# Optimization experiments

Hardware: AMD Instinct MI355X
Metric: run time of the kernel (lower is better)

Reference implementation:

```python
import jax, jax.numpy as jnp
import numpy as np

N, HW, CI = 16, 16384, 2
DIM, DEPTH, CO = 256, 4, 3
OMEGA = 30.0
E = CI * DIM + DIM + DEPTH * (DIM * DIM + DIM)  # 263936


def setup_inputs() -> dict:
    key = jax.random.key(0)
    ks = jax.random.split(key, 8)
    x = jax.random.normal(ks[0], (N, HW, CI), jnp.float32)
    weight_offset = jax.random.normal(ks[1], (N, E), jnp.float32) * 0.01
    # layer 0: uniform(-1/ch_in, 1/ch_in); hidden: uniform(-sqrt(6/dim), sqrt(6/dim)); biases zero
    v0 = 1.0 / CI
    w0 = jax.random.uniform(ks[2], (CI, DIM), jnp.float32, -v0, v0)
    b0 = jnp.zeros((DIM,), jnp.float32)
    vh = float(np.sqrt(6.0 / DIM))
    ws_h = jax.random.uniform(ks[3], (DEPTH, DIM, DIM), jnp.float32, -vh, vh)
    bs_h = jnp.zeros((DEPTH, DIM), jnp.float32)
    # output Linear (torch default init bound 1/sqrt(fan_in)); stored as [DIM, CO]
    lim = float(1.0 / np.sqrt(DIM))
    w_out = jax.random.uniform(ks[4], (DIM, CO), jnp.float32, -lim, lim)
    b_out = jax.random.uniform(ks[5], (CO,), jnp.float32, -lim, lim)
    out_scale = jnp.ones((CO,), jnp.float32)  # output_scale coeff = 1.0
    return {"x": x, "weight_offset": weight_offset, "w0": w0, "b0": b0,
            "ws_h": ws_h, "bs_h": bs_h, "w_out": w_out, "b_out": b_out,
            "out_scale": out_scale}


def reference(x, weight_offset, w0, b0, ws_h, bs_h, w_out, b_out, out_scale):
    n = x.shape[0]
    i = CI * DIM
    ow0 = weight_offset[:, :i].reshape(n, CI, DIM)      # [N, CI, DIM]
    ob0 = weight_offset[:, i:i + DIM]                   # [N, DIM]
    i += DIM
    # first layer: per-sample weight = base + offset, then sin(omega * .)
    h = jnp.einsum('nhc,ncd->nhd', x, w0[None] + ow0) + (b0[None] + ob0)[:, None, :]
    h = jnp.sin(OMEGA * h)
    for l in range(DEPTH):
        ow = weight_offset[:, i:i + DIM * DIM].reshape(n, DIM, DIM)
        i += DIM * DIM
        ob = weight_offset[:, i:i + DIM]
        i += DIM
        h = jnp.einsum('nhd,nde->nhe', h, ws_h[l][None] + ow) + (bs_h[l][None] + ob)[:, None, :]
        h = jnp.sin(h)
    return (h @ w_out + b_out) * out_scale
```

## Files before the change

kernel.cpp:

```cpp
#include <hip/hip_runtime.h>


#define N_S 16
#define HW_S 16384
#define E_S 263936
#define INV2PI 0.15915494309189535f
#define OM2PI  4.774648292756860f

typedef _Float16 f16x8 __attribute__((ext_vector_type(8)));
typedef _Float16 f16x4 __attribute__((ext_vector_type(4)));
typedef _Float16 f16x2 __attribute__((ext_vector_type(2)));
typedef float f32x4 __attribute__((ext_vector_type(4)));

#define WT_OFF   0u
#define W0T_OFF  8388608u
#define B0_OFF   8421376u
#define BE_OFF   8437760u

__device__ __forceinline__ float fsin(float z) {
  return __builtin_amdgcn_sinf(__builtin_amdgcn_fractf(z));
}

__global__ __launch_bounds__(256) void siren_pre(
    const float* __restrict__ wo, const float* __restrict__ w0,
    const float* __restrict__ b0, const float* __restrict__ wsh,
    const float* __restrict__ bsh, char* __restrict__ ws)
{
  __shared__ float tile[64][65];
  int b = blockIdx.x, t = threadIdx.x;
  if (b < 1024) {
    int n = b >> 6, rem = b & 63, l = rem >> 4, sub = rem & 15;
    int tk = sub >> 2, te = sub & 3;
    int e_loc = t & 63, ksub = t >> 6;
    const float* wo_n = wo + (size_t)n * E_S + 768 + l * 65792;
    const float* wsh_l = wsh + l * 65536;
    for (int r = 0; r < 16; ++r) {
      int k_loc = ksub * 16 + r;
      int k = tk * 64 + k_loc, e = te * 64 + e_loc;
      tile[k_loc][e_loc] = (wsh_l[k * 256 + e] + wo_n[k * 256 + e]) * INV2PI;
    }
    __syncthreads();
    _Float16* wtl = (_Float16*)(ws + WT_OFF) + (size_t)(n * 4 + l) * 65536;
    int kp = (t & 31) * 2, esub = t >> 5;
    for (int r = 0; r < 8; ++r) {
      int e_loc2 = esub * 8 + r;
      f16x2 hv;
      hv[0] = (_Float16)tile[kp][e_loc2];
      hv[1] = (_Float16)tile[kp + 1][e_loc2];
      int e = te * 64 + e_loc2, k = tk * 64 + kp;
      int c = k >> 5, kin = k & 31;
      *(f16x2*)(wtl + (size_t)c * 8192 + e * 32 + kin) = hv;
    }
  } else if (b == 1024) {
    float* w0t = (float*)(ws + W0T_OFF);
    float* b0e = (float*)(ws + B0_OFF);
    for (int idx = t; idx < 4096; idx += 256) {
      int n = idx >> 8, e = idx & 255;
      const float* wo_n = wo + (size_t)n * E_S;
      float2 v;
      v.x = (w0[e] + wo_n[e]) * OM2PI;
      v.y = (w0[256 + e] + wo_n[256 + e]) * OM2PI;
      *(float2*)(w0t + (n * 256 + e) * 2) = v;
      b0e[n * 256 + e] = (b0[e] + wo_n[512 + e]) * OM2PI;
    }
  } else {
    float* be = (float*)(ws + BE_OFF);
    for (int idx = t; idx < 16384; idx += 256) {
      int n = idx >> 10, rem = idx & 1023, l = rem >> 8, e = rem & 255;
      be[(n * 4 + l) * 256 + e] =
          (bsh[l * 256 + e] + wo[(size_t)n * E_S + 768 + l * 65792 + 65536 + e]) * INV2PI;
    }
  }
}

__global__ __launch_bounds__(256, 2) void siren_main(
    const float* __restrict__ x, const char* __restrict__ ws,
    const float* __restrict__ w_out, const float* __restrict__ b_out,
    const float* __restrict__ out_scale, float* __restrict__ out)
{
  __shared__ __align__(16) unsigned char sH[65536];
  __shared__ float sWf[768];
  __shared__ float sRed[2][128][3];
  __shared__ float sFin[384];

  int tid = threadIdx.x;
  int lane = tid & 63, wave = tid >> 6;
  int g = lane >> 4, li = lane & 15;
  int we = wave & 1, wp = wave >> 1;
  int bid = blockIdx.x;
  int n = bid & 15, tile = bid >> 4;

  const char* wt_n = ws + WT_OFF + (size_t)n * 524288;

  for (int i = tid; i < 768; i += 256) sWf[i] = w_out[i];

  {
    const float* xp = x + ((size_t)n * HW_S + (size_t)tile * 128) * 2;
    int p = tid & 127;
    float2 xv = *(const float2*)(xp + p * 2);
    const float* w0t = (const float*)(ws + W0T_OFF) + n * 512;
    const float* b0e = (const float*)(ws + B0_OFF) + n * 256;
    int swz = (p & 7) << 4;
    unsigned char* hrow = sH + p * 512;
#pragma unroll
    for (int it = 0; it < 16; ++it) {
      int eg = (tid >> 7) * 16 + it;
      int e0 = eg * 8;
      f32x4 wa = *(const f32x4*)(w0t + e0 * 2);
      f32x4 wb = *(const f32x4*)(w0t + e0 * 2 + 4);
      f32x4 wc = *(const f32x4*)(w0t + e0 * 2 + 8);
      f32x4 wd = *(const f32x4*)(w0t + e0 * 2 + 12);
      f32x4 ba = *(const f32x4*)(b0e + e0);
      f32x4 bb = *(const f32x4*)(b0e + e0 + 4);
      f16x8 hv;
      hv[0] = (_Float16)fsin(fmaf(xv.y, wa[1], fmaf(xv.x, wa[0], ba[0])));
      hv[1] = (_Float16)fsin(fmaf(xv.y, wa[3], fmaf(xv.x, wa[2], ba[1])));
      hv[2] = (_Float16)fsin(fmaf(xv.y, wb[1], fmaf(xv.x, wb[0], ba[2])));
      hv[3] = (_Float16)fsin(fmaf(xv.y, wb[3], fmaf(xv.x, wb[2], ba[3])));
      hv[4] = (_Float16)fsin(fmaf(xv.y, wc[1], fmaf(xv.x, wc[0], bb[0])));
      hv[5] = (_Float16)fsin(fmaf(xv.y, wc[3], fmaf(xv.x, wc[2], bb[1])));
      hv[6] = (_Float16)fsin(fmaf(xv.y, wd[1], fmaf(xv.x, wd[0], bb[2])));
      hv[7] = (_Float16)fsin(fmaf(xv.y, wd[3], fmaf(xv.x, wd[2], bb[3])));
      *(f16x8*)(hrow + ((eg * 16) ^ swz)) = hv;
    }
  }
  __syncthreads();

  const float* be_n = (const float*)(ws + BE_OFF) + n * 1024;
  int laneoff = (we * 128 + li) * 64 + g * 16;
  f32x4 acc[8][4];

  for (int l = 0; l < 4; ++l) {
    const float* bias = be_n + l * 256;
#pragma unroll
    for (int et = 0; et < 8; ++et) {
      f32x4 bv = *(const f32x4*)(bias + we * 128 + et * 16 + g * 4);
#pragma unroll
      for (int pt = 0; pt < 4; ++pt) acc[et][pt] = bv;
    }
    const char* wl = wt_n + (size_t)l * 131072 + laneoff;
#pragma unroll
    for (int c = 0; c < 8; ++c) {
      f16x8 afr[8], bfr[4];
#pragma unroll
      for (int et = 0; et < 8; ++et)
        afr[et] = *(const f16x8*)(wl + c * 16384 + et * 1024);
#pragma unroll
      for (int pt = 0; pt < 4; ++pt) {
        int p = wp * 64 + pt * 16 + li;
        bfr[pt] = *(const f16x8*)(sH + p * 512 + ((c * 64 + g * 16) ^ ((p & 7) << 4)));
      }
#pragma unroll
      for (int et = 0; et < 8; ++et)
#pragma unroll
        for (int pt = 0; pt < 4; ++pt)
          acc[et][pt] = __builtin_amdgcn_mfma_f32_16x16x32_f16(afr[et], bfr[pt], acc[et][pt], 0, 0, 0);
    }
    if (l < 3) {
      __syncthreads();
#pragma unroll
      for (int et = 0; et < 8; ++et) {
        int eb = we * 256 + et * 32 + g * 8;
#pragma unroll
        for (int pt = 0; pt < 4; ++pt) {
          int p = wp * 64 + pt * 16 + li;
          f16x4 hv;
#pragma unroll
          for (int r = 0; r < 4; ++r)
            hv[r] = (_Float16)fsin(acc[et][pt][r]);
          *(f16x4*)(sH + p * 512 + (eb ^ ((p & 7) << 4))) = hv;
        }
      }
      __syncthreads();
    }
  }

  float part[4][3];
#pragma unroll
  for (int pt = 0; pt < 4; ++pt)
#pragma unroll
    for (int co = 0; co < 3; ++co) part[pt][co] = 0.f;
#pragma unroll
  for (int et = 0; et < 8; ++et) {
#pragma unroll
    for (int r = 0; r < 4; ++r) {
      int e = we * 128 + et * 16 + g * 4 + r;
      float wc0 = sWf[e * 3 + 0], wc1 = sWf[e * 3 + 1], wc2 = sWf[e * 3 + 2];
#pragma unroll
      for (int pt = 0; pt < 4; ++pt) {
        float h = fsin(acc[et][pt][r]);
        part[pt][0] = fmaf(h, wc0, part[pt][0]);
        part[pt][1] = fmaf(h, wc1, part[pt][1]);
        part[pt][2] = fmaf(h, wc2, part[pt][2]);
      }
    }
  }
#pragma unroll
  for (int pt = 0; pt < 4; ++pt)
#pragma unroll
    for (int co = 0; co < 3; ++co) {
      float v = part[pt][co];
      v += __shfl_xor(v, 16);
      v += __shfl_xor(v, 32);
      part[pt][co] = v;
    }
  if (g == 0) {
#pragma unroll
    for (int pt = 0; pt < 4; ++pt) {
      int p = wp * 64 + pt * 16 + li;
#pragma unroll
      for (int co = 0; co < 3; ++co)
        sRed[we][p][co] = part[pt][co];
    }
  }
  __syncthreads();
  if (tid < 128) {
    int p = tid;
#pragma unroll
    for (int co = 0; co < 3; ++co)
      sFin[p * 3 + co] = (sRed[0][p][co] + sRed[1][p][co] +
                          b_out[co]) * out_scale[co];
  }
  __syncthreads();
  float* op = out + ((size_t)n * HW_S + (size_t)tile * 128) * 3;
  for (int i = tid; i < 384; i += 256) op[i] = sFin[i];
}

extern "C" void kernel_launch(void* const* d_in, const int* in_sizes, int n_in,
                              void* d_out, int out_size, void* d_ws, size_t ws_size,
                              hipStream_t stream) {
  const float* x      = (const float*)d_in[0];
  const float* wo     = (const float*)d_in[1];
  const float* w0     = (const float*)d_in[2];
  const float* b0     = (const float*)d_in[3];
  const float* wsh    = (const float*)d_in[4];
  const float* bsh    = (const float*)d_in[5];
  const float* w_out  = (const float*)d_in[6];
  const float* b_out  = (const float*)d_in[7];
  const float* oscale = (const float*)d_in[8];
  float* out = (float*)d_out;
  char* ws = (char*)d_ws;

  siren_pre<<<1026, 256, 0, stream>>>(wo, w0, b0, wsh, bsh, ws);
  siren_main<<<2048, 256, 0, stream>>>(x, ws, w_out, b_out, oscale, out);
}
```

Measured before the change: 200.5 us.

## Switch hidden layers to 32x32x16 MFMA with per-wave output-column split

```diff
diff --git a/kernel.cpp b/kernel.cpp
--- a/kernel.cpp
+++ b/kernel.cpp
@@ -11,6 +11,7 @@
 typedef _Float16 f16x4 __attribute__((ext_vector_type(4)));
 typedef _Float16 f16x2 __attribute__((ext_vector_type(2)));
 typedef float f32x4 __attribute__((ext_vector_type(4)));
+typedef float f32x16 __attribute__((ext_vector_type(16)));
 
 #define WT_OFF   0u
 #define W0T_OFF  8388608u
@@ -80,13 +81,12 @@
 {
   __shared__ __align__(16) unsigned char sH[65536];
   __shared__ float sWf[768];
-  __shared__ float sRed[2][128][3];
+  __shared__ float sRed[4][128][3];
   __shared__ float sFin[384];
 
   int tid = threadIdx.x;
-  int lane = tid & 63, wave = tid >> 6;
-  int g = lane >> 4, li = lane & 15;
-  int we = wave & 1, wp = wave >> 1;
+  int lane = tid & 63, eq = tid >> 6;
+  int l31 = lane & 31, lh = lane >> 5;
   int bid = blockIdx.x;
   int n = bid & 15, tile = bid >> 4;
 
@@ -100,7 +100,7 @@
     float2 xv = *(const float2*)(xp + p * 2);
     const float* w0t = (const float*)(ws + W0T_OFF) + n * 512;
     const float* b0e = (const float*)(ws + B0_OFF) + n * 256;
-    int swz = (p & 7) << 4;
+    int swz = (p & 3) << 4;
     unsigned char* hrow = sH + p * 512;
 #pragma unroll
     for (int it = 0; it < 16; ++it) {
@@ -127,90 +127,118 @@
   __syncthreads();
 
   const float* be_n = (const float*)(ws + BE_OFF) + n * 1024;
-  int laneoff = (we * 128 + li) * 64 + g * 16;
-  f32x4 acc[8][4];
+
+  const unsigned char* wp =
+      (const unsigned char*)wt_n + (eq * 64 + l31) * 64 + lh * 16;
+
+  int t4 = ((lh ^ (lane & 1)) << 4);
+  const unsigned char* hb0 = sH + l31 * 512 + t4 + ((0 ^ ((lane >> 1) & 1)) << 5);
+  const unsigned char* hb1 = sH + l31 * 512 + t4 + ((1 ^ ((lane >> 1) & 1)) << 5);
+
+  int S = (lane & 3) << 4;
+  int wbase = l31 * 512 + eq * 128 + lh * 8;
+
+  f32x16 acc[2][4];
+  f16x8 a0, a1, a2, a3, n0, n1, n2, n3;
+  a0 = *(const f16x8*)(wp + 0);
+  a1 = *(const f16x8*)(wp + 32);
+  a2 = *(const f16x8*)(wp + 2048);
+  a3 = *(const f16x8*)(wp + 2080);
 
   for (int l = 0; l < 4; ++l) {
-    const float* bias = be_n + l * 256;
-#pragma unroll
-    for (int et = 0; et < 8; ++et) {
-      f32x4 bv = *(const f32x4*)(bias + we * 128 + et * 16 + g * 4);
-#pragma unroll
-      for (int pt = 0; pt < 4; ++pt) acc[et][pt] = bv;
-    }
-    const char* wl = wt_n + (size_t)l * 131072 + laneoff;
+    const float* bias = be_n + l * 256 + eq * 64 + lh * 4;
+#pragma unroll
+    for (int et = 0; et < 2; ++et) {
+#pragma unroll
+      for (int q = 0; q < 4; ++q) {
+        f32x4 bv = *(const f32x4*)(bias + et * 32 + q * 8);
+#pragma unroll
+        for (int j = 0; j < 4; ++j) {
+#pragma unroll
+          for (int pt = 0; pt < 4; ++pt) acc[et][pt][q * 4 + j] = bv[j];
+        }
+      }
+    }
 #pragma unroll
     for (int c = 0; c < 8; ++c) {
-      f16x8 afr[8], bfr[4];
-#pragma unroll
-      for (int et = 0; et < 8; ++et)
-        afr[et] = *(const f16x8*)(wl + c * 16384 + et * 1024);
+      if (c < 7 || l < 3) {
+        wp += 16384;
+        n0 = *(const f16x8*)(wp + 0);
+        n1 = *(const f16x8*)(wp + 32);
+        n2 = *(const f16x8*)(wp + 2048);
+        n3 = *(const f16x8*)(wp + 2080);
+      }
+      f16x8 b0f[4], b1f[4];
 #pragma unroll
       for (int pt = 0; pt < 4; ++pt) {
-        int p = wp * 64 + pt * 16 + li;
-        bfr[pt] = *(const f16x8*)(sH + p * 512 + ((c * 64 + g * 16) ^ ((p & 7) << 4)));
-      }
-#pragma unroll
-      for (int et = 0; et < 8; ++et)
-#pragma unroll
-        for (int pt = 0; pt < 4; ++pt)
-          acc[et][pt] = __builtin_amdgcn_mfma_f32_16x16x32_f16(afr[et], bfr[pt], acc[et][pt], 0, 0, 0);
+        b0f[pt] = *(const f16x8*)(hb0 + pt * 16384 + c * 64);
+        b1f[pt] = *(const f16x8*)(hb1 + pt * 16384 + c * 64);
+      }
+#pragma unroll
+      for (int pt = 0; pt < 4; ++pt) {
+        acc[0][pt] = __builtin_amdgcn_mfma_f32_32x32x16_f16(a0, b0f[pt], acc[0][pt], 0, 0, 0);
+        acc[0][pt] = __builtin_amdgcn_mfma_f32_32x32x16_f16(a1, b1f[pt], acc[0][pt], 0, 0, 0);
+        acc[1][pt] = __builtin_amdgcn_mfma_f32_32x32x16_f16(a2, b0f[pt], acc[1][pt], 0, 0, 0);
+        acc[1][pt] = __builtin_amdgcn_mfma_f32_32x32x16_f16(a3, b1f[pt], acc[1][pt], 0, 0, 0);
+      }
+      a0 = n0; a1 = n1; a2 = n2; a3 = n3;
     }
     if (l < 3) {
       __syncthreads();
 #pragma unroll
-      for (int et = 0; et < 8; ++et) {
-        int eb = we * 256 + et * 32 + g * 8;
+      for (int et = 0; et < 2; ++et) {
+#pragma unroll
+        for (int q = 0; q < 4; ++q) {
+          int off = wbase + et * 64 + ((q * 16) ^ S);
+#pragma unroll
+          for (int pt = 0; pt < 4; ++pt) {
+            f16x4 hv;
+#pragma unroll
+            for (int j = 0; j < 4; ++j)
+              hv[j] = (_Float16)fsin(acc[et][pt][q * 4 + j]);
+            *(f16x4*)(sH + pt * 16384 + off) = hv;
+          }
+        }
+      }
+      __syncthreads();
+    }
+  }
+
+  float part[4][3];
+#pragma unroll
+  for (int pt = 0; pt < 4; ++pt)
+#pragma unroll
+    for (int co = 0; co < 3; ++co) part[pt][co] = 0.f;
+#pragma unroll
+  for (int et = 0; et < 2; ++et) {
+#pragma unroll
+    for (int q = 0; q < 4; ++q) {
+#pragma unroll
+      for (int j = 0; j < 4; ++j) {
+        int e = eq * 64 + et * 32 + q * 8 + lh * 4 + j;
+        float wc0 = sWf[e * 3 + 0], wc1 = sWf[e * 3 + 1], wc2 = sWf[e * 3 + 2];
 #pragma unroll
         for (int pt = 0; pt < 4; ++pt) {
-          int p = wp * 64 + pt * 16 + li;
-          f16x4 hv;
-#pragma unroll
-          for (int r = 0; r < 4; ++r)
-            hv[r] = (_Float16)fsin(acc[et][pt][r]);
-          *(f16x4*)(sH + p * 512 + (eb ^ ((p & 7) << 4))) = hv;
+          float h = fsin(acc[et][pt][q * 4 + j]);
+          part[pt][0] = fmaf(h, wc0, part[pt][0]);
+          part[pt][1] = fmaf(h, wc1, part[pt][1]);
+          part[pt][2] = fmaf(h, wc2, part[pt][2]);
         }
       }
-      __syncthreads();
-    }
-  }
-
-  float part[4][3];
+    }
+  }
 #pragma unroll
   for (int pt = 0; pt < 4; ++pt)
 #pragma unroll
-    for (int co = 0; co < 3; ++co) part[pt][co] = 0.f;
-#pragma unroll
-  for (int et = 0; et < 8; ++et) {
-#pragma unroll
-    for (int r = 0; r < 4; ++r) {
-      int e = we * 128 + et * 16 + g * 4 + r;
-      float wc0 = sWf[e * 3 + 0], wc1 = sWf[e * 3 + 1], wc2 = sWf[e * 3 + 2];
-#pragma unroll
-      for (int pt = 0; pt < 4; ++pt) {
-        float h = fsin(acc[et][pt][r]);
-        part[pt][0] = fmaf(h, wc0, part[pt][0]);
-        part[pt][1] = fmaf(h, wc1, part[pt][1]);
-        part[pt][2] = fmaf(h, wc2, part[pt][2]);
-      }
-    }
-  }
-#pragma unroll
-  for (int pt = 0; pt < 4; ++pt)
-#pragma unroll
-    for (int co = 0; co < 3; ++co) {
-      float v = part[pt][co];
-      v += __shfl_xor(v, 16);
-      v += __shfl_xor(v, 32);
-      part[pt][co] = v;
-    }
-  if (g == 0) {
+    for (int co = 0; co < 3; ++co)
+      part[pt][co] += __shfl_xor(part[pt][co], 32);
+  if (lane < 32) {
 #pragma unroll
     for (int pt = 0; pt < 4; ++pt) {
-      int p = wp * 64 + pt * 16 + li;
+      int p = pt * 32 + l31;
 #pragma unroll
       for (int co = 0; co < 3; ++co)
-        sRed[we][p][co] = part[pt][co];
+        sRed[eq][p][co] = part[pt][co];
     }
   }
   __syncthreads();
@@ -219,6 +247,7 @@
 #pragma unroll
     for (int co = 0; co < 3; ++co)
       sFin[p * 3 + co] = (sRed[0][p][co] + sRed[1][p][co] +
+                          sRed[2][p][co] + sRed[3][p][co] +
                           b_out[co]) * out_scale[co];
   }
   __syncthreads();
```

After: 180.4 us. 1.11x faster.
